# Kernel tuning notes

Measured on AMD Instinct MI355X. Metric: run time of the kernel, lower is better.

## Reference

```python
import jax, jax.numpy as jnp
import numpy as np

B, C, F, D = 128, 16, 128, 512


def setup_inputs() -> dict:
    key = jax.random.key(0)
    k1, k2 = jax.random.split(key)
    return {
        "c_feats": jax.random.normal(k1, (B, C, D), dtype=jnp.float32),
        "f_feats": jax.random.normal(k2, (B, F, D), dtype=jnp.float32),
    }


def _dtw_path_masks(S):
    """S: [P, c, f] per-pair similarity. Returns [P, c, f] 0/1 max-path masks.

    DP: D[i,j] = max(D[i-1,j], D[i,j-1], D[i-1,j-1]) + S[i-1,j-1], D[0,0]=0,
    borders -inf. Tie-break priority (up, left, diag) matches Python max().
    Row recurrence is vectorized: D[i,j] = Csum[j] + cummax_k<=j(A[k]-Csum[k-1])
    where A[k]=max(D[i-1,k], D[i-1,k-1]) (wavefront-free row-parallel form).
    """
    P_, c, f = S.shape
    NEG = -jnp.inf

    init = jnp.concatenate([jnp.zeros((P_, 1), S.dtype),
                            jnp.full((P_, f), NEG, S.dtype)], axis=1)  # D[0, 0..f]

    def row_step(prev, dt_row):
        # prev: [P, f+1] = D[i-1, 0..f]; dt_row: [P, f] = S[i-1, :]
        A = jnp.maximum(prev[:, 1:], prev[:, :-1])                  # max(D[i-1,j], D[i-1,j-1])
        Ccum = jnp.cumsum(dt_row, axis=1)
        Cm1 = jnp.concatenate([jnp.zeros((P_, 1), dt_row.dtype), Ccum[:, :-1]], axis=1)
        row = Ccum + jax.lax.cummax(A - Cm1, axis=1)                # D[i, 1..f]
        new_prev = jnp.concatenate([jnp.full((P_, 1), NEG, dt_row.dtype), row], axis=1)
        return new_prev, new_prev

    _, rows = jax.lax.scan(row_step, init, jnp.moveaxis(S, 1, 0))   # [c, P, f+1]
    Dm = jnp.moveaxis(jnp.concatenate([init[None], rows], axis=0), 1, 0)  # [P, c+1, f+1]

    # Predecessor choice per cell; argmax picks first max -> priority up,left,diag
    up = Dm[:, :-1, 1:]
    left = Dm[:, 1:, :-1]
    diag = Dm[:, :-1, :-1]
    mv = jnp.argmax(jnp.stack([up, left, diag], axis=-1), axis=-1).astype(jnp.int32)
    mv = jnp.pad(mv, ((0, 0), (1, 0), (1, 0)))                      # [P, c+1, f+1]

    pidx = jnp.arange(P_)

    def bt_step(carry, _):
        mask, i, j = carry
        active = (i > 0) | (j > 0)
        mask = mask.at[pidx, i - 1, j - 1].add(jnp.where(active, 1.0, 0.0).astype(mask.dtype))
        m = mv[pidx, i, j]
        di = jnp.where(m == 1, 0, 1)   # left keeps i
        dj = jnp.where(m == 0, 0, 1)   # up keeps j
        i = jnp.where(active, i - di, i)
        j = jnp.where(active, j - dj, j)
        return (mask, i, j), None

    mask0 = jnp.zeros((P_, c, f), jnp.float32)
    i0 = jnp.full((P_,), c, jnp.int32)
    j0 = jnp.full((P_,), f, jnp.int32)
    (mask, _, _), _ = jax.lax.scan(bt_step, (mask0, i0, j0), None, length=c + f)
    return mask


def reference(c_feats, f_feats):
    b, c, d = c_feats.shape
    f = f_feats.shape[1]
    xn = c_feats / jnp.linalg.norm(c_feats, axis=-1, keepdims=True)
    yn = f_feats / jnp.linalg.norm(f_feats, axis=-1, keepdims=True)
    # Source quirk: y row j is normalized only once outer index i reaches it
    # (y[i-1] bug), so S[i,j] uses normalized y[j] iff j <= i, raw y[j] otherwise.
    Sn = jnp.einsum('mcd,nfd->mncf', xn, yn)
    Sr = jnp.einsum('mcd,nfd->mncf', xn, f_feats)
    tri = jnp.arange(f)[None, :] <= jnp.arange(c)[:, None]          # [c, f]: j <= i
    S = jnp.where(tri, Sn, Sr).reshape(b * b, c, f)
    return _dtw_path_masks(S).reshape(b, b, c, f)
```

## Files before the change

### kernel.cpp

```cpp
#include <hip/hip_runtime.h>
#include <stdint.h>

#define M_TOT 2048
#define N_TOT 16384
#define K_TOT 512

typedef _Float16 f16x8 __attribute__((ext_vector_type(8)));
typedef float f32x16 __attribute__((ext_vector_type(16)));

#define AS1 __attribute__((address_space(1)))
#define AS3 __attribute__((address_space(3)))

__device__ __forceinline__ void ld_lds16(const void* g, void* l) {
    __builtin_amdgcn_global_load_lds((const AS1 void*)g, (AS3 void*)l, 16, 0, 0);
}

__device__ __forceinline__ void split4(float x0, float x1, float x2, float x3,
                                       uint2* hs, uint2* ls) {
    union U { _Float16 h[4]; uint2 u; } H, L;
    _Float16 h0 = (_Float16)x0; H.h[0] = h0; L.h[0] = (_Float16)(x0 - (float)h0);
    _Float16 h1 = (_Float16)x1; H.h[1] = h1; L.h[1] = (_Float16)(x1 - (float)h1);
    _Float16 h2 = (_Float16)x2; H.h[2] = h2; L.h[2] = (_Float16)(x2 - (float)h2);
    _Float16 h3 = (_Float16)x3; H.h[3] = h3; L.h[3] = (_Float16)(x3 - (float)h3);
    *hs = H.u; *ls = L.u;
}

__global__ __launch_bounds__(256) void norm_split_kernel(
    const float* __restrict__ c_feats, const float* __restrict__ f_feats,
    _Float16* __restrict__ Ah, _Float16* __restrict__ Al,
    _Float16* __restrict__ Bh, _Float16* __restrict__ Bl,
    float* __restrict__ normf)
{
    int wave = blockIdx.x * 4 + (threadIdx.x >> 6);
    int lane = threadIdx.x & 63;
    if (wave < 2048) {
        const float* row = c_feats + (size_t)wave * K_TOT;
        float4 v0 = ((const float4*)row)[lane];
        float4 v1 = ((const float4*)row)[lane + 64];
        double ss = (double)v0.x * v0.x + (double)v0.y * v0.y +
                    (double)v0.z * v0.z + (double)v0.w * v0.w +
                    (double)v1.x * v1.x + (double)v1.y * v1.y +
                    (double)v1.z * v1.z + (double)v1.w * v1.w;
        #pragma unroll
        for (int off = 32; off; off >>= 1) ss += __shfl_down(ss, off);
        double tot = __shfl(ss, 0);
        float nrm = sqrtf((float)tot);
        float a0 = v0.x / nrm, a1 = v0.y / nrm, a2 = v0.z / nrm, a3 = v0.w / nrm;
        float b0 = v1.x / nrm, b1 = v1.y / nrm, b2 = v1.z / nrm, b3 = v1.w / nrm;
        uint2 h, l;
        split4(a0, a1, a2, a3, &h, &l);
        ((uint2*)(Ah + (size_t)wave * K_TOT))[lane] = h;
        ((uint2*)(Al + (size_t)wave * K_TOT))[lane] = l;
        split4(b0, b1, b2, b3, &h, &l);
        ((uint2*)(Ah + (size_t)wave * K_TOT))[lane + 64] = h;
        ((uint2*)(Al + (size_t)wave * K_TOT))[lane + 64] = l;
    } else if (wave < 18432) {
        int fr = wave - 2048;
        const float* row = f_feats + (size_t)fr * K_TOT;
        float4 v0 = ((const float4*)row)[lane];
        float4 v1 = ((const float4*)row)[lane + 64];
        double ss = (double)v0.x * v0.x + (double)v0.y * v0.y +
                    (double)v0.z * v0.z + (double)v0.w * v0.w +
                    (double)v1.x * v1.x + (double)v1.y * v1.y +
                    (double)v1.z * v1.z + (double)v1.w * v1.w;
        #pragma unroll
        for (int off = 32; off; off >>= 1) ss += __shfl_down(ss, off);
        if (lane == 0) normf[fr] = sqrtf((float)ss);
        uint2 h, l;
        split4(v0.x, v0.y, v0.z, v0.w, &h, &l);
        ((uint2*)(Bh + (size_t)fr * K_TOT))[lane] = h;
        ((uint2*)(Bl + (size_t)fr * K_TOT))[lane] = l;
        split4(v1.x, v1.y, v1.z, v1.w, &h, &l);
        ((uint2*)(Bh + (size_t)fr * K_TOT))[lane + 64] = h;
        ((uint2*)(Bl + (size_t)fr * K_TOT))[lane + 64] = l;
    }
}

#define SRS 130
#define SPS 2096

__device__ __forceinline__ float dpp_shr1_f32(float x) {
    union { float f; int i; } u, v;
    u.f = x;
    v.i = __builtin_amdgcn_update_dpp(u.i, u.i, 0x111, 0xF, 0xF, false);
    return v.f;
}

__global__ __launch_bounds__(256, 2) void gemm_dtw_kernel(
    const _Float16* __restrict__ Ah, const _Float16* __restrict__ Al,
    const _Float16* __restrict__ Bh, const _Float16* __restrict__ Bl,
    const float* __restrict__ normf,
    float* __restrict__ out)
{
    __shared__ __attribute__((aligned(16))) float S[8 * SPS];
    __shared__ uint32_t mv[8][132];
    __shared__ int bounds[8][16];

    _Float16* const sAh = (_Float16*)S;
    _Float16* const sAl = sAh + 128 * 32;
    _Float16* const sBh = sAl + 128 * 32;
    _Float16* const sBl = sBh + 128 * 32;

    const int t = threadIdx.x;
    const int w = t >> 6, lane = t & 63;
    const int ntile = ((blockIdx.x & 7) << 4) | (blockIdx.x >> 3);
    const int gm0 = blockIdx.y * 128, gn0 = ntile * 128;
    const int wm = (w & 1) * 64, wn = (w >> 1) * 64;
    const int m32 = lane & 31;
    const int kql0 = lane >> 5;

    f32x16 acc[2][2] = {};
    const int l0 = w * 128 + lane;

    for (int k0 = 0; k0 < K_TOT; k0 += 32) {
        #pragma unroll
        for (int c = 0; c < 2; ++c) {
            int l = l0 + c * 64;
            int lrow = l >> 2, kq = l & 3;
            int kqs = kq ^ ((lrow >> 1) & 3);
            size_t goffA = (size_t)(gm0 + lrow) * K_TOT + k0 + kqs * 8;
            size_t goffB = (size_t)(gn0 + lrow) * K_TOT + k0 + kqs * 8;
            ld_lds16(Ah + goffA, sAh + (size_t)l * 8);
            ld_lds16(Al + goffA, sAl + (size_t)l * 8);
            ld_lds16(Bh + goffB, sBh + (size_t)l * 8);
            ld_lds16(Bl + goffB, sBl + (size_t)l * 8);
        }
        __syncthreads();

        #pragma unroll
        for (int kh = 0; kh < 2; ++kh) {
            f16x8 fah[2], fal[2], fbh[2], fbl[2];
            #pragma unroll
            for (int x = 0; x < 2; ++x) {
                int arr = wm + x * 32 + m32;
                int brr = wn + x * 32 + m32;
                int kqa = (kh * 2 + kql0) ^ ((arr >> 1) & 3);
                int kqb = (kh * 2 + kql0) ^ ((brr >> 1) & 3);
                int ar = arr * 32 + kqa * 8;
                int br = brr * 32 + kqb * 8;
                fah[x] = *(const f16x8*)(sAh + ar);
                fal[x] = *(const f16x8*)(sAl + ar);
                fbh[x] = *(const f16x8*)(sBh + br);
                fbl[x] = *(const f16x8*)(sBl + br);
            }
            #pragma unroll
            for (int mi = 0; mi < 2; ++mi)
                #pragma unroll
                for (int ni = 0; ni < 2; ++ni) {
                    acc[mi][ni] = __builtin_amdgcn_mfma_f32_32x32x16_f16(fah[mi], fbl[ni], acc[mi][ni], 0, 0, 0);
                    acc[mi][ni] = __builtin_amdgcn_mfma_f32_32x32x16_f16(fal[mi], fbh[ni], acc[mi][ni], 0, 0, 0);
                    acc[mi][ni] = __builtin_amdgcn_mfma_f32_32x32x16_f16(fah[mi], fbh[ni], acc[mi][ni], 0, 0, 0);
                }
        }
        __syncthreads();
    }

    const int rq = 4 * kql0;
    #pragma unroll
    for (int ni = 0; ni < 2; ++ni) {
        const int col = wn + ni * 32 + m32;
        const bool cn = (col < 16);
        const float nf = cn ? normf[gn0 + col] : 1.f;
        #pragma unroll
        for (int mi = 0; mi < 2; ++mi) {
            #pragma unroll
            for (int reg = 0; reg < 16; ++reg) {
                const int rg = wm + mi * 32 + (reg & 3) + 8 * (reg >> 2) + rq;
                float v = acc[mi][ni][reg];
                if (cn && col <= (rg & 15)) v /= nf;
                S[(rg >> 4) * SPS + (rg & 15) * SRS + col] = v;
            }
        }
    }
    __syncthreads();

    const int q = lane >> 4, r = lane & 15;
    const bool act = (q < 2);
    const int p = w * 2 + (q & 1);
    const float* Sp = S + p * SPS + r * SRS;
    uint32_t* mvq = &mv[p][0];

    const float NEG = -1e30f;
    float Dp = NEG, rawprev = NEG;
    uint32_t mvbuf = 0;
    int j = -r;
    int svoff = (-r) & 127;

#define DTW_STEP(BOUNDARY)                                                      \
    {                                                                           \
        float upr = dpp_shr1_f32(Dp);                                           \
        float dg = rawprev;                                                     \
        rawprev = upr;                                                          \
        float up = (r == 0) ? NEG : upr;                                        \
        float lf = Dp;                                                          \
        if (BOUNDARY) {                                                         \
            if (j == 0) { lf = NEG; dg = (r == 0) ? 0.0f : NEG; }               \
            else if (r == 0) dg = NEG;                                          \
        } else {                                                                \
            if (r == 0) dg = NEG;                                               \
        }                                                                       \
        float sv = Sp[svoff];                                                   \
        svoff = (svoff + 1) & 127;                                              \
        int m = (up >= lf && up >= dg) ? 0 : ((lf >= dg) ? 1 : 2);              \
        float Dc = fmaxf(up, fmaxf(lf, dg)) + sv;                               \
        if (act && (unsigned)j < 128u) {                                        \
            mvbuf |= (uint32_t)m << (2 * (j & 15));                             \
            if ((j & 15) == 15) { mvq[r * 8 + (j >> 4)] = mvbuf; mvbuf = 0; }   \
        }                                                                       \
        Dp = Dc;                                                                \
        ++j;                                                                    \
    }

    #pragma unroll
    for (int tt = 0; tt < 16; ++tt) DTW_STEP(true)
    #pragma unroll
    for (int tt = 16; tt < 143; ++tt) DTW_STEP(false)
#undef DTW_STEP

    if (r == 0 && act) {
        int i = 16, jj = 128, hic = 127;
        int cidx = -1;
        uint32_t word = 0;
        for (int it = 0; it < 160; ++it) {
            if (i <= 0) break;
            int idx = (i - 1) * 8 + ((jj - 1) >> 4);
            if (idx != cidx) { word = mvq[idx]; cidx = idx; }
            int m = (int)((word >> (2 * ((jj - 1) & 15))) & 3u);
            if (m == 1) { --jj; continue; }
            bounds[p][i - 1] = (jj - 1) | (hic << 8);
            if (m == 2) --jj;
            --i;
            hic = jj - 1;
        }
    }

    const int nn = ntile;
    const int mmb = gm0 >> 4;
    #pragma unroll 4
    for (int it = 0; it < 16; ++it) {
        int flat = it * 64 + lane;
        int q2 = flat >> 9;
        int rem = flat & 511;
        int ii = rem >> 5;
        int c4 = rem & 31;
        int b = bounds[w * 2 + q2][ii];
        int lo = b & 0xff, hi = (b >> 8) & 0xff;
        int j0 = c4 * 4;
        float4 v;
        v.x = (j0 + 0 >= lo && j0 + 0 <= hi) ? 1.f : 0.f;
        v.y = (j0 + 1 >= lo && j0 + 1 <= hi) ? 1.f : 0.f;
        v.z = (j0 + 2 >= lo && j0 + 2 <= hi) ? 1.f : 0.f;
        v.w = (j0 + 3 >= lo && j0 + 3 <= hi) ? 1.f : 0.f;
        float* tb = out + ((size_t)((mmb + w * 2 + q2) * 128 + nn)) * 2048;
        *(float4*)(tb + ii * 128 + j0) = v;
    }
}

extern "C" void kernel_launch(void* const* d_in, const int* in_sizes, int n_in,
                              void* d_out, int out_size, void* d_ws, size_t ws_size,
                              hipStream_t stream)
{
    const float* c_feats = (const float*)d_in[0];
    const float* f_feats = (const float*)d_in[1];
    float* out = (float*)d_out;

    _Float16* Ah = (_Float16*)d_ws;
    _Float16* Al = Ah + (size_t)M_TOT * K_TOT;
    _Float16* Bh = Al + (size_t)M_TOT * K_TOT;
    _Float16* Bl = Bh + (size_t)N_TOT * K_TOT;
    float* normf = (float*)(Bl + (size_t)N_TOT * K_TOT);

    norm_split_kernel<<<4608, 256, 0, stream>>>(c_feats, f_feats, Ah, Al, Bh, Bl, normf);
    dim3 g(N_TOT / 128, M_TOT / 128);
    gemm_dtw_kernel<<<g, 256, 0, stream>>>(Ah, Al, Bh, Bl, normf, out);
}
```

Before: 370.8 us.

## Skew S tile layout and run DTW with four pairs per wave in two waves

The S staging tile is stored with each row shifted by its row index, so each lane in the anti-diagonal wavefront reads consecutive elements. That allows the lane to prefetch S as float4 vector loads from LDS instead of scalar loads with modular offsets. The DTW work is reassigned so only waves 0 and 1 run it, with all 64 lanes covering four pairs each instead of two pairs per wave across eight waves. A barrier is added before the mask write. The trade-off is fewer waves doing serial DP work, which may hurt latency hiding, plus a larger LDS footprint that could lower occupancy.

```diff
diff --git a/kernel.cpp b/kernel.cpp
--- a/kernel.cpp
+++ b/kernel.cpp
@@ -6,6 +6,7 @@
 #define K_TOT 512
 
 typedef _Float16 f16x8 __attribute__((ext_vector_type(8)));
+typedef float f32x4 __attribute__((ext_vector_type(4)));
 typedef float f32x16 __attribute__((ext_vector_type(16)));
 
 #define AS1 __attribute__((address_space(1)))
@@ -76,8 +77,8 @@
     }
 }
 
-#define SRS 130
-#define SPS 2096
+#define SRS 148
+#define SPS 2368
 
 __device__ __forceinline__ float dpp_shr1_f32(float x) {
     union { float f; int i; } u, v;
@@ -166,44 +167,46 @@
             #pragma unroll
             for (int reg = 0; reg < 16; ++reg) {
                 const int rg = wm + mi * 32 + (reg & 3) + 8 * (reg >> 2) + rq;
+                const int rr = rg & 15;
                 float v = acc[mi][ni][reg];
-                if (cn && col <= (rg & 15)) v /= nf;
-                S[(rg >> 4) * SPS + (rg & 15) * SRS + col] = v;
+                if (cn && col <= rr) v /= nf;
+                S[(rg >> 4) * SPS + rr * SRS + col + rr] = v;
             }
         }
     }
     __syncthreads();
 
     const int q = lane >> 4, r = lane & 15;
-    const bool act = (q < 2);
-    const int p = w * 2 + (q & 1);
-    const float* Sp = S + p * SPS + r * SRS;
-    uint32_t* mvq = &mv[p][0];
-
-    const float NEG = -1e30f;
-    float Dp = NEG, rawprev = NEG;
-    uint32_t mvbuf = 0;
-    int j = -r;
-    int svoff = (-r) & 127;
-
-#define DTW_STEP(BOUNDARY)                                                      \
+    if (w < 2) {
+        const int p = w * 4 + q;
+        const float* Sp = S + p * SPS + r * SRS;
+        uint32_t* mvq = &mv[p][0];
+
+        const float NEG = -1e30f;
+        float Dp = NEG, rawprev = NEG;
+        uint32_t mvbuf = 0;
+        int j = -r;
+
+        f32x4 ch[4];
+        #pragma unroll
+        for (int c0 = 0; c0 < 4; ++c0) ch[c0] = *(const f32x4*)(Sp + 4 * c0);
+
+#define DTW_STEP(T, SV)                                                         \
     {                                                                           \
         float upr = dpp_shr1_f32(Dp);                                           \
         float dg = rawprev;                                                     \
         rawprev = upr;                                                          \
         float up = (r == 0) ? NEG : upr;                                        \
         float lf = Dp;                                                          \
-        if (BOUNDARY) {                                                         \
+        if ((T) < 16) {                                                         \
             if (j == 0) { lf = NEG; dg = (r == 0) ? 0.0f : NEG; }               \
             else if (r == 0) dg = NEG;                                          \
         } else {                                                                \
             if (r == 0) dg = NEG;                                               \
         }                                                                       \
-        float sv = Sp[svoff];                                                   \
-        svoff = (svoff + 1) & 127;                                              \
         int m = (up >= lf && up >= dg) ? 0 : ((lf >= dg) ? 1 : 2);              \
-        float Dc = fmaxf(up, fmaxf(lf, dg)) + sv;                               \
-        if (act && (unsigned)j < 128u) {                                        \
+        float Dc = fmaxf(up, fmaxf(lf, dg)) + (SV);                             \
+        if ((unsigned)j < 128u) {                                               \
             mvbuf |= (uint32_t)m << (2 * (j & 15));                             \
             if ((j & 15) == 15) { mvq[r * 8 + (j >> 4)] = mvbuf; mvbuf = 0; }   \
         }                                                                       \
@@ -211,28 +214,36 @@
         ++j;                                                                    \
     }
 
-    #pragma unroll
-    for (int tt = 0; tt < 16; ++tt) DTW_STEP(true)
-    #pragma unroll
-    for (int tt = 16; tt < 143; ++tt) DTW_STEP(false)
+        #pragma unroll
+        for (int g = 0; g < 36; ++g) {
+            f32x4 cur = ch[g & 3];
+            if (g + 4 < 36) ch[g & 3] = *(const f32x4*)(Sp + 4 * (g + 4));
+            #pragma unroll
+            for (int e = 0; e < 4; ++e) {
+                const int T = g * 4 + e;
+                if (T < 143) DTW_STEP(T, cur[e])
+            }
+        }
 #undef DTW_STEP
 
-    if (r == 0 && act) {
-        int i = 16, jj = 128, hic = 127;
-        int cidx = -1;
-        uint32_t word = 0;
-        for (int it = 0; it < 160; ++it) {
-            if (i <= 0) break;
-            int idx = (i - 1) * 8 + ((jj - 1) >> 4);
-            if (idx != cidx) { word = mvq[idx]; cidx = idx; }
-            int m = (int)((word >> (2 * ((jj - 1) & 15))) & 3u);
-            if (m == 1) { --jj; continue; }
-            bounds[p][i - 1] = (jj - 1) | (hic << 8);
-            if (m == 2) --jj;
-            --i;
-            hic = jj - 1;
-        }
-    }
+        if (r == 0) {
+            int i = 16, jj = 128, hic = 127;
+            int cidx = -1;
+            uint32_t word = 0;
+            for (int it = 0; it < 160; ++it) {
+                if (i <= 0) break;
+                int idx = (i - 1) * 8 + ((jj - 1) >> 4);
+                if (idx != cidx) { word = mvq[idx]; cidx = idx; }
+                int m = (int)((word >> (2 * ((jj - 1) & 15))) & 3u);
+                if (m == 1) { --jj; continue; }
+                bounds[p][i - 1] = (jj - 1) | (hic << 8);
+                if (m == 2) --jj;
+                --i;
+                hic = jj - 1;
+            }
+        }
+    }
+    __syncthreads();
 
     const int nn = ntile;
     const int mmb = gm0 >> 4;
```

Result: no change. 371.2 us (+0.1%).
